# Kernel tuning notes

Hardware: AMD Instinct MI355X
Metric: run time of the kernel (lower is better)

The kernel has to match this reference:

```python
import jax, jax.numpy as jnp
import numpy as np

I, H, L, O = 11, 33, 3, 18

def lstm_layer(x_tbi, W_ih, W_hh, b_ih, b_hh):
    # x_tbi: [T, B, in]; W_ih: [4H, in]; W_hh: [4H, H]
    T, B = x_tbi.shape[0], x_tbi.shape[1]
    # precompute input contribution for all timesteps (one big GEMM)
    xg = jnp.einsum('tbi,gi->tbg', x_tbi, W_ih) + b_ih + b_hh  # [T, B, 4H]
    h0 = jnp.zeros((B, H), x_tbi.dtype)
    c0 = jnp.zeros((B, H), x_tbi.dtype)

    def step(carry, xg_t):
        h, c = carry
        gates = xg_t + h @ W_hh.T                      # [B, 4H]
        i, f, g, o = jnp.split(gates, 4, axis=-1)      # PyTorch gate order i,f,g,o
        i = jax.nn.sigmoid(i)
        f = jax.nn.sigmoid(f)
        g = jnp.tanh(g)
        o = jax.nn.sigmoid(o)
        c = f * c + i * g
        h = o * jnp.tanh(c)
        return (h, c), h

    (hT, cT), ys = jax.lax.scan(step, (h0, c0), xg)
    return ys, hT, cT  # ys: [T, B, H]


def setup_inputs() -> dict:
    key = jax.random.key(0)
    ks = jax.random.split(key, 20)
    B, T = 512, 2048
    s = 1.0 / np.sqrt(H)
    d = {'x': jax.random.normal(ks[0], (B, T, I), jnp.float32)}
    in_sizes = [I, H, H]
    for l in range(L):
        d[f'W_ih{l}'] = jax.random.uniform(ks[1 + 4 * l], (4 * H, in_sizes[l]), jnp.float32, -s, s)
        d[f'W_hh{l}'] = jax.random.uniform(ks[2 + 4 * l], (4 * H, H), jnp.float32, -s, s)
        d[f'b_ih{l}'] = jax.random.uniform(ks[3 + 4 * l], (4 * H,), jnp.float32, -s, s)
        d[f'b_hh{l}'] = jax.random.uniform(ks[4 + 4 * l], (4 * H,), jnp.float32, -s, s)
    d['W1'] = jax.random.normal(ks[13], (4 * O, H), jnp.float32) * 0.05
    d['b1'] = jnp.zeros((4 * O,), jnp.float32)
    d['W2'] = jax.random.normal(ks[14], (O, 4 * O), jnp.float32) * 0.05
    d['b2'] = jnp.zeros((O,), jnp.float32)
    return d


def reference(x, W_ih0, W_hh0, b_ih0, b_hh0, W_ih1, W_hh1, b_ih1, b_hh1,
              W_ih2, W_hh2, b_ih2, b_hh2, W1, b1, W2, b2):
    # x: [B, T, I] (batch_first) -> time-major for scan
    xt = jnp.transpose(x, (1, 0, 2))  # [T, B, I]
    params = [(W_ih0, W_hh0, b_ih0, b_hh0),
              (W_ih1, W_hh1, b_ih1, b_hh1),
              (W_ih2, W_hh2, b_ih2, b_hh2)]
    hiddens = []
    cur = xt
    for (Wi, Wh, bi, bh) in params:
        cur, hT, _ = lstm_layer(cur, Wi, Wh, bi, bh)
        hiddens.append(hT)
    hidden = jnp.stack(hiddens, axis=0)  # [L, B, H] (final hidden state per layer)
    # MLP head (dropout inactive at inference); torch nn.GELU default = exact erf
    h1 = jax.nn.gelu(hidden @ W1.T + b1, approximate=False)
    out = h1 @ W2.T + b2  # [L, B, O]
    return out, hidden
```

## Files before the change

kernel.cpp:

```cpp
#include <hip/hip_runtime.h>
#include <math.h>

#define TT 2048
#define BB 512
#define II 11
#define HH 33
#define NL 3
#define OO 18
#define HSLOT 48
#define XPAD 16

typedef _Float16 h2 __attribute__((ext_vector_type(2)));
typedef _Float16 h8 __attribute__((ext_vector_type(8)));

__device__ __forceinline__ float sigm_f(float x) {
    float e = __expf(-x);
    return __builtin_amdgcn_rcpf(1.0f + e);
}
__device__ __forceinline__ float tanh_f(float x) {
    float e = __expf(2.0f * x);
    return 1.0f - 2.0f * __builtin_amdgcn_rcpf(e + 1.0f);
}

__device__ __forceinline__ h8 gldh8(const float* p, int k0, int rem) {
    h8 v;
    #pragma unroll
    for (int i = 0; i < 8; ++i) v[i] = (_Float16)((k0 + i < rem) ? p[k0 + i] : 0.0f);
    return v;
}
__device__ __forceinline__ h2 gldh2(const float* p, int k0, int rem) {
    h2 v;
    v.x = (_Float16)((k0 + 0 < rem) ? p[k0 + 0] : 0.0f);
    v.y = (_Float16)((k0 + 1 < rem) ? p[k0 + 1] : 0.0f);
    return v;
}

#define FD(a, p, q) a = __builtin_amdgcn_fdot2((p), (q), a, false)
#define DUO(vi_, vo_, SEL) do { \
    FD(a0i, (vi_).SEL, (xw0).SEL); FD(a1i, (vi_).SEL, (xw1).SEL); \
    FD(a2i, (vi_).SEL, (xw2).SEL); FD(a3i, (vi_).SEL, (xw3).SEL); \
    FD(a0h, (vo_).SEL, (hw0).SEL); FD(a1h, (vo_).SEL, (hw1).SEL); \
    FD(a2h, (vo_).SEL, (hw2).SEL); FD(a3h, (vo_).SEL, (hw3).SEL); } while (0)
#define DUOQ(vi_, vo_, xq0, xq1, xq2, xq3, hq0, hq1, hq2, hq3) do { \
    const h8 xw0 = (xq0), xw1 = (xq1), xw2 = (xq2), xw3 = (xq3); \
    const h8 hw0 = (hq0), hw1 = (hq1), hw2 = (hq2), hw3 = (hq3); \
    DUO(vi_, vo_, s01); DUO(vi_, vo_, s23); \
    DUO(vi_, vo_, s45); DUO(vi_, vo_, s67); } while (0)

__global__ __launch_bounds__(128, 1) void lstm_pipeline_kernel(
    const float* __restrict__ x,
    const float* __restrict__ Wih0, const float* __restrict__ Whh0,
    const float* __restrict__ bih0, const float* __restrict__ bhh0,
    const float* __restrict__ Wih1, const float* __restrict__ Whh1,
    const float* __restrict__ bih1, const float* __restrict__ bhh1,
    const float* __restrict__ Wih2, const float* __restrict__ Whh2,
    const float* __restrict__ bih2, const float* __restrict__ bhh2,
    const float* __restrict__ W1, const float* __restrict__ b1,
    const float* __restrict__ W2, const float* __restrict__ b2,
    float* __restrict__ hidden_out,
    float* __restrict__ outp)
{
    __shared__ __align__(16) _Float16 xst[TT + 2][XPAD];
    __shared__ __align__(16) _Float16 buf[2][NL + 1][HSLOT];
    __shared__ float hfin[NL][HH + 1];
    __shared__ float h1s[NL][4 * OO];

    const int tid = threadIdx.x;
    const int bg  = blockIdx.x;

    for (int i = tid; i < 2 * (NL + 1) * HSLOT; i += 128)
        ((_Float16*)buf)[i] = (_Float16)0.0f;

    for (int f = tid; f < (TT + 2) * XPAD; f += 128) {
        const int i = f & (XPAD - 1);
        const int t = f >> 4;
        if (i >= II || t >= TT) ((_Float16*)xst)[f] = (_Float16)0.0f;
    }
    {
        const float* xblk = x + (size_t)bg * TT * II;
        const float4* xf4 = (const float4*)xblk;
        for (int f4 = tid; f4 < (TT * II) / 4; f4 += 128) {
            const float4 v = xf4[f4];
            const int e0 = 4 * f4;
            #pragma unroll
            for (int e = 0; e < 4; ++e) {
                const int idx = e0 + e;
                const int t = idx / II;
                const int i = idx - t * II;
                xst[t][i] = (_Float16)((&v.x)[e]);
            }
        }
    }

    const bool comp = (tid < 99);
    const int  u    = tid;
    const int  l    = (u < 33) ? 0 : (u < 66) ? 1 : 2;
    const int  j    = u - 33 * l;

    h8 z8 = {0,0,0,0,0,0,0,0};
    h2 z2 = {(_Float16)0.0f, (_Float16)0.0f};
    h8 x00=z8,x01=z8,x02=z8,x03=z8; h2 x0t=z2;
    h8 x10=z8,x11=z8,x12=z8,x13=z8; h2 x1t=z2;
    h8 x20=z8,x21=z8,x22=z8,x23=z8; h2 x2t=z2;
    h8 x30=z8,x31=z8,x32=z8,x33=z8; h2 x3t=z2;
    h8 h00=z8,h01=z8,h02=z8,h03=z8; h2 h0t=z2;
    h8 h10=z8,h11=z8,h12=z8,h13=z8; h2 h1t=z2;
    h8 h20=z8,h21=z8,h22=z8,h23=z8; h2 h2t=z2;
    h8 h30=z8,h31=z8,h32=z8,h33=z8; h2 h3t=z2;
    float b0 = 0.0f, b1v = 0.0f, b2v = 0.0f, b3v = 0.0f;

    if (comp) {
        const float* bip = (l == 0) ? bih0 : (l == 1) ? bih1 : bih2;
        const float* bhp = (l == 0) ? bhh0 : (l == 1) ? bhh1 : bhh2;
        b0  = bip[0 * HH + j] + bhp[0 * HH + j];
        b1v = bip[1 * HH + j] + bhp[1 * HH + j];
        b2v = bip[2 * HH + j] + bhp[2 * HH + j];
        b3v = bip[3 * HH + j] + bhp[3 * HH + j];

        const float* Wi = (l == 0) ? Wih0 : (l == 1) ? Wih1 : Wih2;
        const float* Wh = (l == 0) ? Whh0 : (l == 1) ? Whh1 : Whh2;
        const int kin = (l == 0) ? II : HH;
        const float* r0 = Wi + (0 * HH + j) * kin;
        const float* r1 = Wi + (1 * HH + j) * kin;
        const float* r2 = Wi + (2 * HH + j) * kin;
        const float* r3 = Wi + (3 * HH + j) * kin;
        x00=gldh8(r0,0,kin); x01=gldh8(r0,8,kin); x02=gldh8(r0,16,kin); x03=gldh8(r0,24,kin); x0t=gldh2(r0,32,kin);
        x10=gldh8(r1,0,kin); x11=gldh8(r1,8,kin); x12=gldh8(r1,16,kin); x13=gldh8(r1,24,kin); x1t=gldh2(r1,32,kin);
        x20=gldh8(r2,0,kin); x21=gldh8(r2,8,kin); x22=gldh8(r2,16,kin); x23=gldh8(r2,24,kin); x2t=gldh2(r2,32,kin);
        x30=gldh8(r3,0,kin); x31=gldh8(r3,8,kin); x32=gldh8(r3,16,kin); x33=gldh8(r3,24,kin); x3t=gldh2(r3,32,kin);
        const float* s0 = Wh + (0 * HH + j) * HH;
        const float* s1 = Wh + (1 * HH + j) * HH;
        const float* s2 = Wh + (2 * HH + j) * HH;
        const float* s3 = Wh + (3 * HH + j) * HH;
        h00=gldh8(s0,0,HH); h01=gldh8(s0,8,HH); h02=gldh8(s0,16,HH); h03=gldh8(s0,24,HH); h0t=gldh2(s0,32,HH);
        h10=gldh8(s1,0,HH); h11=gldh8(s1,8,HH); h12=gldh8(s1,16,HH); h13=gldh8(s1,24,HH); h1t=gldh2(s1,32,HH);
        h20=gldh8(s2,0,HH); h21=gldh8(s2,8,HH); h22=gldh8(s2,16,HH); h23=gldh8(s2,24,HH); h2t=gldh2(s2,32,HH);
        h30=gldh8(s3,0,HH); h31=gldh8(s3,8,HH); h32=gldh8(s3,16,HH); h33=gldh8(s3,24,HH); h3t=gldh2(s3,32,HH);
    }

    __syncthreads();

    float c = 0.0f;

    const _Float16* rin[2]  = { &buf[0][l][0],     &buf[1][l][0] };
    const _Float16* rown[2] = { &buf[0][l + 1][0], &buf[1][l + 1][0] };
    _Float16*       wrp[2]  = { &buf[0][l + 1][j], &buf[1][l + 1][j] };
    const _Float16* xst0    = &xst[0][0];

    auto step = [&](int s, int rp, bool check, bool out)
        __attribute__((always_inline)) {
        const int wp = rp ^ 1;
        const bool active = check ? (comp && (s >= l) && (s - l < TT)) : comp;
        if (active) {
            const _Float16* ri = (l == 0) ? (xst0 + (s << 4)) : rin[rp];
            const h8* VI = (const h8*)ri;
            const h8 vi0 = VI[0], vi1 = VI[1], vi2 = VI[2], vi3 = VI[3];
            const h2 vit = *(const h2*)(ri + 32);
            const h8* VO = (const h8*)rown[rp];
            const h8 vo0 = VO[0], vo1 = VO[1], vo2 = VO[2], vo3 = VO[3];
            const h2 vot = *(const h2*)(rown[rp] + 32);

            float a0i = b0, a1i = b1v, a2i = b2v, a3i = b3v;
            float a0h = 0.0f, a1h = 0.0f, a2h = 0.0f, a3h = 0.0f;
            DUOQ(vi0, vo0, x00, x10, x20, x30, h00, h10, h20, h30);
            DUOQ(vi1, vo1, x01, x11, x21, x31, h01, h11, h21, h31);
            DUOQ(vi2, vo2, x02, x12, x22, x32, h02, h12, h22, h32);
            DUOQ(vi3, vo3, x03, x13, x23, x33, h03, h13, h23, h33);
            FD(a0i, vit, x0t); FD(a1i, vit, x1t);
            FD(a2i, vit, x2t); FD(a3i, vit, x3t);
            FD(a0h, vot, h0t); FD(a1h, vot, h1t);
            FD(a2h, vot, h2t); FD(a3h, vot, h3t);

            const float s0 = a0i + a0h;
            const float s1 = a1i + a1h;
            const float s2 = a2i + a2h;
            const float s3 = a3i + a3h;

            const float ig = sigm_f(s0);
            const float fg = sigm_f(s1);
            const float gg = tanh_f(s2);
            const float og = sigm_f(s3);
            c = __builtin_fmaf(fg, c, ig * gg);
            const float hnew = og * tanh_f(c);

            *wrp[wp] = (_Float16)hnew;
            if (out && (s - l == TT - 1)) {
                hidden_out[((size_t)l * BB + bg) * HH + j] = hnew;
                hfin[l][j] = hnew;
            }
        }
        __syncthreads();
    };

    step(0, 0, true, false);
    step(1, 1, true, false);
    for (int s = 2; s < TT - 4; s += 2) {
        step(s,     0, false, false);
        step(s + 1, 1, false, false);
    }
    step(TT - 4, 0, false, false);
    step(TT - 3, 1, false, false);
    step(TT - 2, 0, false, false);
    step(TT - 1, 1, false, true);
    step(TT,     0, true,  true);
    step(TT + 1, 1, true,  true);

    if (tid < 4 * OO) {
        #pragma unroll
        for (int ml = 0; ml < NL; ++ml) {
            float a = b1[tid];
            #pragma unroll
            for (int k = 0; k < HH; ++k) a += hfin[ml][k] * W1[tid * HH + k];
            h1s[ml][tid] = 0.5f * a * (1.0f + erff(a * 0.70710678118654752f));
        }
    }
    __syncthreads();
    if (tid < NL * OO) {
        const int ol = tid / OO, o = tid % OO;
        float a = b2[o];
        #pragma unroll
        for (int m = 0; m < 4 * OO; ++m) a += h1s[ol][m] * W2[o * (4 * OO) + m];
        outp[((size_t)ol * BB + bg) * OO + o] = a;
    }
}

extern "C" void kernel_launch(void* const* d_in, const int* in_sizes, int n_in,
                              void* d_out, int out_size, void* d_ws, size_t ws_size,
                              hipStream_t stream) {
    const float* x    = (const float*)d_in[0];
    const float* Wih0 = (const float*)d_in[1];
    const float* Whh0 = (const float*)d_in[2];
    const float* bih0 = (const float*)d_in[3];
    const float* bhh0 = (const float*)d_in[4];
    const float* Wih1 = (const float*)d_in[5];
    const float* Whh1 = (const float*)d_in[6];
    const float* bih1 = (const float*)d_in[7];
    const float* bhh1 = (const float*)d_in[8];
    const float* Wih2 = (const float*)d_in[9];
    const float* Whh2 = (const float*)d_in[10];
    const float* bih2 = (const float*)d_in[11];
    const float* bhh2 = (const float*)d_in[12];
    const float* W1   = (const float*)d_in[13];
    const float* b1   = (const float*)d_in[14];
    const float* W2   = (const float*)d_in[15];
    const float* b2   = (const float*)d_in[16];

    float* out    = (float*)d_out;
    float* hidden = out + NL * BB * OO;

    lstm_pipeline_kernel<<<BB, 128, 0, stream>>>(
        x, Wih0, Whh0, bih0, bhh0, Wih1, Whh1, bih1, bhh1,
        Wih2, Whh2, bih2, bhh2, W1, b1, W2, b2, hidden, out);
}
```

Measured before the change: 1.039 ms.

## Process two batch elements per block to interleave independent recurrences

```diff
diff --git a/kernel.cpp b/kernel.cpp
--- a/kernel.cpp
+++ b/kernel.cpp
@@ -60,24 +60,27 @@
     float* __restrict__ hidden_out,
     float* __restrict__ outp)
 {
-    __shared__ __align__(16) _Float16 xst[TT + 2][XPAD];
-    __shared__ __align__(16) _Float16 buf[2][NL + 1][HSLOT];
-    __shared__ float hfin[NL][HH + 1];
-    __shared__ float h1s[NL][4 * OO];
+    __shared__ __align__(16) _Float16 xst[2][TT + 2][XPAD];
+    __shared__ __align__(16) _Float16 buf[2][2][NL + 1][HSLOT];
+    __shared__ float hfin[2][NL][HH + 1];
+    __shared__ float h1s[2][NL][4 * OO];
 
     const int tid = threadIdx.x;
-    const int bg  = blockIdx.x;
-
-    for (int i = tid; i < 2 * (NL + 1) * HSLOT; i += 128)
+    const int bgA = blockIdx.x;
+    const int bgB = blockIdx.x + 256;
+
+    for (int i = tid; i < 2 * 2 * (NL + 1) * HSLOT; i += 128)
         ((_Float16*)buf)[i] = (_Float16)0.0f;
 
-    for (int f = tid; f < (TT + 2) * XPAD; f += 128) {
+    for (int f = tid; f < 2 * (TT + 2) * XPAD; f += 128) {
         const int i = f & (XPAD - 1);
-        const int t = f >> 4;
+        int t = f >> 4;
+        if (t >= (TT + 2)) t -= (TT + 2);
         if (i >= II || t >= TT) ((_Float16*)xst)[f] = (_Float16)0.0f;
     }
-    {
-        const float* xblk = x + (size_t)bg * TT * II;
+    #pragma unroll
+    for (int bb = 0; bb < 2; ++bb) {
+        const float* xblk = x + (size_t)(bb ? bgB : bgA) * TT * II;
         const float4* xf4 = (const float4*)xblk;
         for (int f4 = tid; f4 < (TT * II) / 4; f4 += 128) {
             const float4 v = xf4[f4];
@@ -87,7 +90,7 @@
                 const int idx = e0 + e;
                 const int t = idx / II;
                 const int i = idx - t * II;
-                xst[t][i] = (_Float16)((&v.x)[e]);
+                xst[bb][t][i] = (_Float16)((&v.x)[e]);
             }
         }
     }
@@ -140,53 +143,85 @@
 
     __syncthreads();
 
-    float c = 0.0f;
-
-    const _Float16* rin[2]  = { &buf[0][l][0],     &buf[1][l][0] };
-    const _Float16* rown[2] = { &buf[0][l + 1][0], &buf[1][l + 1][0] };
-    _Float16*       wrp[2]  = { &buf[0][l + 1][j], &buf[1][l + 1][j] };
-    const _Float16* xst0    = &xst[0][0];
+    float cA = 0.0f, cB = 0.0f;
+
+    const _Float16* rinA[2]  = { &buf[0][0][l][0],     &buf[0][1][l][0] };
+    const _Float16* rownA[2] = { &buf[0][0][l + 1][0], &buf[0][1][l + 1][0] };
+    _Float16*       wrpA[2]  = { &buf[0][0][l + 1][j], &buf[0][1][l + 1][j] };
+    const _Float16* rinB[2]  = { &buf[1][0][l][0],     &buf[1][1][l][0] };
+    const _Float16* rownB[2] = { &buf[1][0][l + 1][0], &buf[1][1][l + 1][0] };
+    _Float16*       wrpB[2]  = { &buf[1][0][l + 1][j], &buf[1][1][l + 1][j] };
+    const _Float16* xstA = &xst[0][0][0];
+    const _Float16* xstB = &xst[1][0][0];
 
     auto step = [&](int s, int rp, bool check, bool out)
         __attribute__((always_inline)) {
         const int wp = rp ^ 1;
         const bool active = check ? (comp && (s >= l) && (s - l < TT)) : comp;
         if (active) {
-            const _Float16* ri = (l == 0) ? (xst0 + (s << 4)) : rin[rp];
-            const h8* VI = (const h8*)ri;
-            const h8 vi0 = VI[0], vi1 = VI[1], vi2 = VI[2], vi3 = VI[3];
-            const h2 vit = *(const h2*)(ri + 32);
-            const h8* VO = (const h8*)rown[rp];
-            const h8 vo0 = VO[0], vo1 = VO[1], vo2 = VO[2], vo3 = VO[3];
-            const h2 vot = *(const h2*)(rown[rp] + 32);
-
-            float a0i = b0, a1i = b1v, a2i = b2v, a3i = b3v;
-            float a0h = 0.0f, a1h = 0.0f, a2h = 0.0f, a3h = 0.0f;
-            DUOQ(vi0, vo0, x00, x10, x20, x30, h00, h10, h20, h30);
-            DUOQ(vi1, vo1, x01, x11, x21, x31, h01, h11, h21, h31);
-            DUOQ(vi2, vo2, x02, x12, x22, x32, h02, h12, h22, h32);
-            DUOQ(vi3, vo3, x03, x13, x23, x33, h03, h13, h23, h33);
-            FD(a0i, vit, x0t); FD(a1i, vit, x1t);
-            FD(a2i, vit, x2t); FD(a3i, vit, x3t);
-            FD(a0h, vot, h0t); FD(a1h, vot, h1t);
-            FD(a2h, vot, h2t); FD(a3h, vot, h3t);
-
-            const float s0 = a0i + a0h;
-            const float s1 = a1i + a1h;
-            const float s2 = a2i + a2h;
-            const float s3 = a3i + a3h;
-
-            const float ig = sigm_f(s0);
-            const float fg = sigm_f(s1);
-            const float gg = tanh_f(s2);
-            const float og = sigm_f(s3);
-            c = __builtin_fmaf(fg, c, ig * gg);
-            const float hnew = og * tanh_f(c);
-
-            *wrp[wp] = (_Float16)hnew;
+            float sA0, sA1, sA2, sA3, sB0, sB1, sB2, sB3;
+            {
+                const _Float16* ri = (l == 0) ? (xstA + (s << 4)) : rinA[rp];
+                const h8* VI = (const h8*)ri;
+                const h8 vi0 = VI[0], vi1 = VI[1], vi2 = VI[2], vi3 = VI[3];
+                const h2 vit = *(const h2*)(ri + 32);
+                const h8* VO = (const h8*)rownA[rp];
+                const h8 vo0 = VO[0], vo1 = VO[1], vo2 = VO[2], vo3 = VO[3];
+                const h2 vot = *(const h2*)(rownA[rp] + 32);
+                float a0i = b0, a1i = b1v, a2i = b2v, a3i = b3v;
+                float a0h = 0.0f, a1h = 0.0f, a2h = 0.0f, a3h = 0.0f;
+                DUOQ(vi0, vo0, x00, x10, x20, x30, h00, h10, h20, h30);
+                DUOQ(vi1, vo1, x01, x11, x21, x31, h01, h11, h21, h31);
+                DUOQ(vi2, vo2, x02, x12, x22, x32, h02, h12, h22, h32);
+                DUOQ(vi3, vo3, x03, x13, x23, x33, h03, h13, h23, h33);
+                FD(a0i, vit, x0t); FD(a1i, vit, x1t);
+                FD(a2i, vit, x2t); FD(a3i, vit, x3t);
+                FD(a0h, vot, h0t); FD(a1h, vot, h1t);
+                FD(a2h, vot, h2t); FD(a3h, vot, h3t);
+                sA0 = a0i + a0h; sA1 = a1i + a1h;
+                sA2 = a2i + a2h; sA3 = a3i + a3h;
+            }
+            {
+                const _Float16* ri = (l == 0) ? (xstB + (s << 4)) : rinB[rp];
+                const h8* VI = (const h8*)ri;
+                const h8 vi0 = VI[0], vi1 = VI[1], vi2 = VI[2], vi3 = VI[3];
+                const h2 vit = *(const h2*)(ri + 32);
+                const h8* VO = (const h8*)rownB[rp];
+                const h8 vo0 = VO[0], vo1 = VO[1], vo2 = VO[2], vo3 = VO[3];
+                const h2 vot = *(const h2*)(rownB[rp] + 32);
+                float a0i = b0, a1i = b1v, a2i = b2v, a3i = b3v;
+                float a0h = 0.0f, a1h = 0.0f, a2h = 0.0f, a3h = 0.0f;
+                DUOQ(vi0, vo0, x00, x10, x20, x30, h00, h10, h20, h30);
+                DUOQ(vi1, vo1, x01, x11, x21, x31, h01, h11, h21, h31);
+                DUOQ(vi2, vo2, x02, x12, x22, x32, h02, h12, h22, h32);
+                DUOQ(vi3, vo3, x03, x13, x23, x33, h03, h13, h23, h33);
+                FD(a0i, vit, x0t); FD(a1i, vit, x1t);
+                FD(a2i, vit, x2t); FD(a3i, vit, x3t);
+                FD(a0h, vot, h0t); FD(a1h, vot, h1t);
+                FD(a2h, vot, h2t); FD(a3h, vot, h3t);
+                sB0 = a0i + a0h; sB1 = a1i + a1h;
+                sB2 = a2i + a2h; sB3 = a3i + a3h;
+            }
+            const float igA = sigm_f(sA0);
+            const float fgA = sigm_f(sA1);
+            const float ggA = tanh_f(sA2);
+            const float ogA = sigm_f(sA3);
+            const float igB = sigm_f(sB0);
+            const float fgB = sigm_f(sB1);
+            const float ggB = tanh_f(sB2);
+            const float ogB = sigm_f(sB3);
+            cA = __builtin_fmaf(fgA, cA, igA * ggA);
+            cB = __builtin_fmaf(fgB, cB, igB * ggB);
+            const float hA = ogA * tanh_f(cA);
+            const float hB = ogB * tanh_f(cB);
+
+            *wrpA[wp] = (_Float16)hA;
+            *wrpB[wp] = (_Float16)hB;
             if (out && (s - l == TT - 1)) {
-                hidden_out[((size_t)l * BB + bg) * HH + j] = hnew;
-                hfin[l][j] = hnew;
+                hidden_out[((size_t)l * BB + bgA) * HH + j] = hA;
+                hidden_out[((size_t)l * BB + bgB) * HH + j] = hB;
+                hfin[0][l][j] = hA;
+                hfin[1][l][j] = hB;
             }
         }
         __syncthreads();
@@ -207,20 +242,26 @@
 
     if (tid < 4 * OO) {
         #pragma unroll
-        for (int ml = 0; ml < NL; ++ml) {
-            float a = b1[tid];
+        for (int bb = 0; bb < 2; ++bb) {
             #pragma unroll
-            for (int k = 0; k < HH; ++k) a += hfin[ml][k] * W1[tid * HH + k];
-            h1s[ml][tid] = 0.5f * a * (1.0f + erff(a * 0.70710678118654752f));
+            for (int ml = 0; ml < NL; ++ml) {
+                float a = b1[tid];
+                #pragma unroll
+                for (int k = 0; k < HH; ++k) a += hfin[bb][ml][k] * W1[tid * HH + k];
+                h1s[bb][ml][tid] = 0.5f * a * (1.0f + erff(a * 0.70710678118654752f));
+            }
         }
     }
     __syncthreads();
     if (tid < NL * OO) {
         const int ol = tid / OO, o = tid % OO;
-        float a = b2[o];
         #pragma unroll
-        for (int m = 0; m < 4 * OO; ++m) a += h1s[ol][m] * W2[o * (4 * OO) + m];
-        outp[((size_t)ol * BB + bg) * OO + o] = a;
+        for (int bb = 0; bb < 2; ++bb) {
+            float a = b2[o];
+            #pragma unroll
+            for (int m = 0; m < 4 * OO; ++m) a += h1s[bb][ol][m] * W2[o * (4 * OO) + m];
+            outp[((size_t)ol * BB + (bb ? bgB : bgA)) * OO + o] = a;
+        }
     }
 }
 
@@ -248,7 +289,7 @@
     float* out    = (float*)d_out;
     float* hidden = out + NL * BB * OO;
 
-    lstm_pipeline_kernel<<<BB, 128, 0, stream>>>(
+    lstm_pipeline_kernel<<<BB / 2, 128, 0, stream>>>(
         x, Wih0, Whh0, bih0, bhh0, Wih1, Whh1, bih1, bhh1,
         Wih2, Whh2, bih2, bhh2, W1, b1, W2, b2, hidden, out);
 }
```

Result: slower. 1.798 ms (+73.0%).

## Skew layer wavefront by two steps to prefetch input projection off critical path

Applied to the files above, without the earlier changes.

```diff
diff --git a/kernel.cpp b/kernel.cpp
--- a/kernel.cpp
+++ b/kernel.cpp
@@ -9,6 +9,7 @@
 #define OO 18
 #define HSLOT 48
 #define XPAD 16
+#define XROWS (TT + 8)
 
 typedef _Float16 h2 __attribute__((ext_vector_type(2)));
 typedef _Float16 h8 __attribute__((ext_vector_type(8)));
@@ -36,18 +37,14 @@
 }
 
 #define FD(a, p, q) a = __builtin_amdgcn_fdot2((p), (q), a, false)
-#define DUO(vi_, vo_, SEL) do { \
-    FD(a0i, (vi_).SEL, (xw0).SEL); FD(a1i, (vi_).SEL, (xw1).SEL); \
-    FD(a2i, (vi_).SEL, (xw2).SEL); FD(a3i, (vi_).SEL, (xw3).SEL); \
-    FD(a0h, (vo_).SEL, (hw0).SEL); FD(a1h, (vo_).SEL, (hw1).SEL); \
-    FD(a2h, (vo_).SEL, (hw2).SEL); FD(a3h, (vo_).SEL, (hw3).SEL); } while (0)
-#define DUOQ(vi_, vo_, xq0, xq1, xq2, xq3, hq0, hq1, hq2, hq3) do { \
-    const h8 xw0 = (xq0), xw1 = (xq1), xw2 = (xq2), xw3 = (xq3); \
-    const h8 hw0 = (hq0), hw1 = (hq1), hw2 = (hq2), hw3 = (hq3); \
-    DUO(vi_, vo_, s01); DUO(vi_, vo_, s23); \
-    DUO(vi_, vo_, s45); DUO(vi_, vo_, s67); } while (0)
-
-__global__ __launch_bounds__(128, 1) void lstm_pipeline_kernel(
+#define DQ4X(A0, A1, A2, A3, v, w0, w1, w2, w3) do { \
+    FD(A0,(v).s01,(w0).s01); FD(A1,(v).s01,(w1).s01); FD(A2,(v).s01,(w2).s01); FD(A3,(v).s01,(w3).s01); \
+    FD(A0,(v).s23,(w0).s23); FD(A1,(v).s23,(w1).s23); FD(A2,(v).s23,(w2).s23); FD(A3,(v).s23,(w3).s23); \
+    FD(A0,(v).s45,(w0).s45); FD(A1,(v).s45,(w1).s45); FD(A2,(v).s45,(w2).s45); FD(A3,(v).s45,(w3).s45); \
+    FD(A0,(v).s67,(w0).s67); FD(A1,(v).s67,(w1).s67); FD(A2,(v).s67,(w2).s67); FD(A3,(v).s67,(w3).s67); \
+} while (0)
+
+__global__ __launch_bounds__(128, 1) void lstm_skew2_kernel(
     const float* __restrict__ x,
     const float* __restrict__ Wih0, const float* __restrict__ Whh0,
     const float* __restrict__ bih0, const float* __restrict__ bhh0,
@@ -60,18 +57,18 @@
     float* __restrict__ hidden_out,
     float* __restrict__ outp)
 {
-    __shared__ __align__(16) _Float16 xst[TT + 2][XPAD];
-    __shared__ __align__(16) _Float16 buf[2][NL + 1][HSLOT];
+    __shared__ __align__(16) _Float16 xst[XROWS][XPAD];
+    __shared__ __align__(16) _Float16 buf[3][NL + 1][HSLOT];
     __shared__ float hfin[NL][HH + 1];
     __shared__ float h1s[NL][4 * OO];
 
     const int tid = threadIdx.x;
     const int bg  = blockIdx.x;
 
-    for (int i = tid; i < 2 * (NL + 1) * HSLOT; i += 128)
+    for (int i = tid; i < 3 * (NL + 1) * HSLOT; i += 128)
         ((_Float16*)buf)[i] = (_Float16)0.0f;
 
-    for (int f = tid; f < (TT + 2) * XPAD; f += 128) {
+    for (int f = tid; f < XROWS * XPAD; f += 128) {
         const int i = f & (XPAD - 1);
         const int t = f >> 4;
         if (i >= II || t >= TT) ((_Float16*)xst)[f] = (_Float16)0.0f;
@@ -141,69 +138,100 @@
     __syncthreads();
 
     float c = 0.0f;
-
-    const _Float16* rin[2]  = { &buf[0][l][0],     &buf[1][l][0] };
-    const _Float16* rown[2] = { &buf[0][l + 1][0], &buf[1][l + 1][0] };
-    _Float16*       wrp[2]  = { &buf[0][l + 1][j], &buf[1][l + 1][j] };
-    const _Float16* xst0    = &xst[0][0];
-
-    auto step = [&](int s, int rp, bool check, bool out)
+    float p0 = b0, p1 = b1v, p2 = b2v, p3 = b3v;
+
+    const _Float16* vip[3] = { &buf[0][l][0],     &buf[1][l][0],     &buf[2][l][0] };
+    const _Float16* vop[3] = { &buf[0][l+1][0],   &buf[1][l+1][0],   &buf[2][l+1][0] };
+    _Float16*       wr3[3] = { &buf[0][l+1][j],   &buf[1][l+1][j],   &buf[2][l+1][j] };
+    const _Float16* xst0   = &xst[0][0];
+
+    auto prefetch_in = [&](const _Float16* rn) __attribute__((always_inline)) {
+        const h8* VI = (const h8*)rn;
+        const h8 vi0 = VI[0], vi1 = VI[1], vi2 = VI[2], vi3 = VI[3];
+        const h2 vit = *(const h2*)(rn + 32);
+        float n0 = b0, n1 = b1v, n2 = b2v, n3 = b3v;
+        DQ4X(n0, n1, n2, n3, vi0, x00, x10, x20, x30);
+        DQ4X(n0, n1, n2, n3, vi1, x01, x11, x21, x31);
+        DQ4X(n0, n1, n2, n3, vi2, x02, x12, x22, x32);
+        DQ4X(n0, n1, n2, n3, vi3, x03, x13, x23, x33);
+        FD(n0, vit, x0t); FD(n1, vit, x1t);
+        FD(n2, vit, x2t); FD(n3, vit, x3t);
+        p0 = n0; p1 = n1; p2 = n2; p3 = n3;
+    };
+
+    if (comp) prefetch_in((l == 0) ? xst0 : vip[2]);
+    __syncthreads();
+
+    auto core = [&](int s, int r, bool out) __attribute__((always_inline)) {
+        const _Float16* ro = vop[(r + 2) % 3];
+        const h8* VO = (const h8*)ro;
+        const h8 vo0 = VO[0], vo1 = VO[1], vo2 = VO[2], vo3 = VO[3];
+        const h2 vot = *(const h2*)(ro + 32);
+
+        float o0a=0.f,o1a=0.f,o2a=0.f,o3a=0.f;
+        float o0b=0.f,o1b=0.f,o2b=0.f,o3b=0.f;
+        DQ4X(o0a, o1a, o2a, o3a, vo0, h00, h10, h20, h30);
+        DQ4X(o0a, o1a, o2a, o3a, vo1, h01, h11, h21, h31);
+        DQ4X(o0b, o1b, o2b, o3b, vo2, h02, h12, h22, h32);
+        DQ4X(o0b, o1b, o2b, o3b, vo3, h03, h13, h23, h33);
+        FD(o0b, vot, h0t); FD(o1b, vot, h1t);
+        FD(o2b, vot, h2t); FD(o3b, vot, h3t);
+
+        const float s0 = p0 + (o0a + o0b);
+        const float s1 = p1 + (o1a + o1b);
+        const float s2 = p2 + (o2a + o2b);
+        const float s3 = p3 + (o3a + o3b);
+
+        const float ig = sigm_f(s0);
+        const float fg = sigm_f(s1);
+        const float gg = tanh_f(s2);
+        const float og = sigm_f(s3);
+        c = __builtin_fmaf(fg, c, ig * gg);
+        const float hnew = og * tanh_f(c);
+
+        *wr3[r] = (_Float16)hnew;
+        if (out && (s - 2 * l == TT - 1)) {
+            hidden_out[((size_t)l * BB + bg) * HH + j] = hnew;
+            hfin[l][j] = hnew;
+        }
+    };
+
+    auto step = [&](int s, int r, bool check, bool out)
         __attribute__((always_inline)) {
-        const int wp = rp ^ 1;
-        const bool active = check ? (comp && (s >= l) && (s - l < TT)) : comp;
-        if (active) {
-            const _Float16* ri = (l == 0) ? (xst0 + (s << 4)) : rin[rp];
-            const h8* VI = (const h8*)ri;
-            const h8 vi0 = VI[0], vi1 = VI[1], vi2 = VI[2], vi3 = VI[3];
-            const h2 vit = *(const h2*)(ri + 32);
-            const h8* VO = (const h8*)rown[rp];
-            const h8 vo0 = VO[0], vo1 = VO[1], vo2 = VO[2], vo3 = VO[3];
-            const h2 vot = *(const h2*)(rown[rp] + 32);
-
-            float a0i = b0, a1i = b1v, a2i = b2v, a3i = b3v;
-            float a0h = 0.0f, a1h = 0.0f, a2h = 0.0f, a3h = 0.0f;
-            DUOQ(vi0, vo0, x00, x10, x20, x30, h00, h10, h20, h30);
-            DUOQ(vi1, vo1, x01, x11, x21, x31, h01, h11, h21, h31);
-            DUOQ(vi2, vo2, x02, x12, x22, x32, h02, h12, h22, h32);
-            DUOQ(vi3, vo3, x03, x13, x23, x33, h03, h13, h23, h33);
-            FD(a0i, vit, x0t); FD(a1i, vit, x1t);
-            FD(a2i, vit, x2t); FD(a3i, vit, x3t);
-            FD(a0h, vot, h0t); FD(a1h, vot, h1t);
-            FD(a2h, vot, h2t); FD(a3h, vot, h3t);
-
-            const float s0 = a0i + a0h;
-            const float s1 = a1i + a1h;
-            const float s2 = a2i + a2h;
-            const float s3 = a3i + a3h;
-
-            const float ig = sigm_f(s0);
-            const float fg = sigm_f(s1);
-            const float gg = tanh_f(s2);
-            const float og = sigm_f(s3);
-            c = __builtin_fmaf(fg, c, ig * gg);
-            const float hnew = og * tanh_f(c);
-
-            *wrp[wp] = (_Float16)hnew;
-            if (out && (s - l == TT - 1)) {
-                hidden_out[((size_t)l * BB + bg) * HH + j] = hnew;
-                hfin[l][j] = hnew;
+        if (!check) {
+            if (comp) {
+                core(s, r, false);
+                prefetch_in((l == 0) ? (xst0 + ((s + 1) << 4)) : vip[(r + 2) % 3]);
             }
+        } else {
+            const bool act  = comp && (s >= 2 * l) && (s - 2 * l < TT);
+            const bool nact = comp && (s + 1 >= 2 * l) && (s + 1 - 2 * l < TT);
+            if (act)  core(s, r, out);
+            if (nact) prefetch_in((l == 0) ? (xst0 + ((s + 1) << 4)) : vip[(r + 2) % 3]);
         }
         __syncthreads();
     };
 
     step(0, 0, true, false);
     step(1, 1, true, false);
-    for (int s = 2; s < TT - 4; s += 2) {
+    step(2, 2, true, false);
+    step(3, 0, true, false);
+    step(4, 1, true, false);
+    step(5, 2, true, false);
+    for (int s = 6; s < 2046; s += 6) {
         step(s,     0, false, false);
         step(s + 1, 1, false, false);
-    }
-    step(TT - 4, 0, false, false);
-    step(TT - 3, 1, false, false);
-    step(TT - 2, 0, false, false);
-    step(TT - 1, 1, false, true);
-    step(TT,     0, true,  true);
-    step(TT + 1, 1, true,  true);
+        step(s + 2, 2, false, false);
+        step(s + 3, 0, false, false);
+        step(s + 4, 1, false, false);
+        step(s + 5, 2, false, false);
+    }
+    step(2046, 0, true, true);
+    step(2047, 1, true, true);
+    step(2048, 2, true, true);
+    step(2049, 0, true, true);
+    step(2050, 1, true, true);
+    step(2051, 2, true, true);
 
     if (tid < 4 * OO) {
         #pragma unroll
@@ -248,7 +276,7 @@
     float* out    = (float*)d_out;
     float* hidden = out + NL * BB * OO;
 
-    lstm_pipeline_kernel<<<BB, 128, 0, stream>>>(
+    lstm_skew2_kernel<<<BB, 128, 0, stream>>>(
         x, Wih0, Whh0, bih0, bhh0, Wih1, Whh1, bih1, bhh1,
         Wih2, Whh2, bih2, bhh2, W1, b1, W2, b2, hidden, out);
 }
```

Measured after the change: 1.087 ms. 4.6% more time.
